# Kernel tuning notes

Measured on AMD Instinct MI355X. Metric: run time of the kernel, lower is better.

## Reference

```python
import jax, jax.numpy as jnp
import numpy as np
from jax import lax

DN = ('NDHWC', 'DHWIO', 'NDHWC')
SHAPE = (33, 33, 33)
B = 2
N = 40000
C = 64


def setup_inputs() -> dict:
    key = jax.random.key(0)
    ks = jax.random.split(key, 24)
    D, H, W = SHAPE
    # unique active voxel coords (batch, z, y, x)
    rng = np.random.default_rng(0)
    idx = rng.choice(B * D * H * W, size=N, replace=False)
    b = idx // (D * H * W)
    r = idx % (D * H * W)
    coors = np.stack([b, r // (H * W), (r // W) % H, r % W], axis=1).astype(np.int32)

    def w(k, shape, scale=0.1):
        return jax.random.normal(k, shape, jnp.float32) * scale

    inp = {
        'features': jax.random.normal(ks[0], (N, 3), jnp.float32),
        'coors': jnp.asarray(coors),
        'batch_size': B,
        'w1': w(ks[1], (3, 3, 3, 3, C), 0.2), 'b1': w(ks[2], (C,), 0.05),
        'w2': w(ks[3], (3, 3, 3, C, C), 0.05), 'b2': w(ks[4], (C,), 0.05),
        'w3': w(ks[5], (3, 3, 3, C, C), 0.05), 'b3': w(ks[6], (C,), 0.05),
        'wt': w(ks[7], (3, 3, 3, C, C), 0.05), 'bt': w(ks[8], (C,), 0.05),
        'w5': w(ks[9], (3, 3, 3, C, C), 0.05), 'b5': w(ks[10], (C,), 0.05),
    }
    # folded eval-mode BatchNorm: y = x*s + h  (s = gamma/sqrt(var+eps), h = beta - mean*s)
    for i, (sk, hk) in enumerate(zip(ks[11:16], ks[16:21]), start=1):
        inp[f's{i}'] = 1.0 + 0.1 * jax.random.normal(sk, (C,), jnp.float32)
        inp[f'h{i}'] = 0.05 * jax.random.normal(hk, (C,), jnp.float32)
    return inp


def _forward(features, coors, batch_size,
             w1, b1, w2, b2, w3, b3, wt, bt, w5, b5,
             s1, h1, s2, h2, s3, h3, s4, h4, s5, h5):
    D, H, W = SHAPE
    bi, zi, yi, xi = coors[:, 0], coors[:, 1], coors[:, 2], coors[:, 3]
    # densify SparseConvTensor (zeros at inactive sites) + active mask
    x = jnp.zeros((batch_size, D, H, W, features.shape[-1]), features.dtype)
    x = x.at[bi, zi, yi, xi].set(features)
    m = jnp.zeros((batch_size, D, H, W, 1), jnp.float32).at[bi, zi, yi, xi].set(1.0)
    ones3 = jnp.ones((3, 3, 3, 1, 1), jnp.float32)

    conv = lambda a, k, pad: lax.conv_general_dilated(a, k, (1, 1, 1), pad, dimension_numbers=DN)
    # masked BN(eval) + ReLU: applied only on active sites, background stays exactly 0
    act = lambda y, mm, s, h: jnp.where(mm, jax.nn.relu(y * s + h), 0.0)

    # SparseConv3d(3,64,3): valid conv; output actives = 1-dilation of input actives
    x = conv(x, w1, 'VALID')
    m1 = conv(m, ones3, 'VALID') > 0  # [B,31,31,31,1]
    x = act(x + b1, m1, s1, h1)

    # two SubMConv3d(64,64,3) sharing indice_key: same active set, SAME padding
    x = act(conv(x, w2, 'SAME') + b2, m1, s2, h2)
    x = act(conv(x, w3, 'SAME') + b3, m1, s3, h3)

    # SparseConvTranspose3d(64,64,3,2): out = (D-1)*2+3; actives = transposed dilation
    x = lax.conv_transpose(x, wt, (2, 2, 2), 'VALID', dimension_numbers=DN)
    mT = lax.conv_transpose(m1.astype(jnp.float32), ones3, (2, 2, 2), 'VALID', dimension_numbers=DN) > 0
    x = act(x + bt, mT, s4, h4)

    # ToDense -> dense Conv3d(64,64,3) -> BN -> ReLU (dense: applied everywhere)
    x = conv(x, w5, 'VALID') + b5
    x = jax.nn.relu(x * s5 + h5)
    return jnp.transpose(x, (0, 4, 1, 2, 3))  # NCDHW like spconv ToDense output


def reference(features, coors, batch_size,
              w1, b1, w2, b2, w3, b3, wt, bt, w5, b5,
              s1, h1, s2, h2, s3, h3, s4, h4, s5, h5):
    return _forward(features, coors, batch_size,
                    w1, b1, w2, b2, w3, b3, wt, bt, w5, b5,
                    s1, h1, s2, h2, s3, h3, s4, h4, s5, h5)
```

## Files before the change

### kernel.cpp

```cpp
#include <hip/hip_runtime.h>
#include <cstdint>

constexpr int BB = 2, C = 64;
constexpr int D1 = 31;
constexpr int DP = 33;
constexpr int D4 = 63;
constexpr int D5 = 61;
constexpr int D5CUBE = D5*D5*D5;

constexpr int NV1 = BB*D1*D1*D1;
constexpr int NVP = BB*DP*DP*DP;
constexpr int NV4 = BB*D4*D4*D4;
constexpr int NV5 = BB*D5*D5*D5;

constexpr size_t alup(size_t x) { return (x + 255) & ~(size_t)255; }
constexpr size_t OB_X0  = 0;
constexpr size_t OB_M0  = alup(OB_X0  + (size_t)NVP*3*4);
constexpr size_t OB_M1P = alup(OB_M0  + (size_t)NVP*4);
constexpr size_t OB_X1  = alup(OB_M1P + (size_t)NVP*4);
constexpr size_t OB_X2  = alup(OB_X1  + (size_t)NVP*64*2);
constexpr size_t OB_X3  = alup(OB_X2  + (size_t)NVP*64*2);
constexpr size_t OB_MT  = alup(OB_X3  + (size_t)NVP*64*2);
constexpr size_t OB_X4  = alup(OB_MT  + (size_t)NV4*4);
constexpr size_t OB_WB2 = alup(OB_X4  + (size_t)NV4*64*2);
constexpr size_t OB_WB3 = alup(OB_WB2 + (size_t)27*64*64*2);
constexpr size_t OB_WBT = alup(OB_WB3 + (size_t)27*64*64*2);
constexpr size_t OB_WB5 = alup(OB_WBT + (size_t)27*64*64*2);

typedef __attribute__((ext_vector_type(8))) short short8;
typedef __attribute__((ext_vector_type(4))) float f32x4;

__device__ inline unsigned short f2bf(float f) {
  unsigned int u = __float_as_uint(f);
  u = (u + 0x7FFFu + ((u >> 16) & 1u)) >> 16;
  return (unsigned short)u;
}

template<int DD>
__device__ inline void decodev(int vox, int& b, int& z, int& y, int& x) {
  x = vox % DD; int r = vox / DD;
  y = r % DD;   r /= DD;
  z = r % DD;   b = r / DD;
}

__device__ inline int xcd_swz(int bid, int nb) {
  int q = nb >> 3, r = nb & 7;
  int xcd = bid & 7, idx = bid >> 3;
  return (xcd < r ? xcd*(q+1) : r*(q+1) + (xcd - r)*q) + idx;
}

__global__ void k_scatter(const float* __restrict__ feat, const int* __restrict__ coors,
                          int n, float* __restrict__ x0, float* __restrict__ m0) {
  int i = blockIdx.x*blockDim.x + threadIdx.x;
  if (i >= n) return;
  int b = coors[4*i+0], z = coors[4*i+1], y = coors[4*i+2], x = coors[4*i+3];
  int v = ((b*DP + z)*DP + y)*DP + x;
  x0[v*3+0] = feat[3*i+0];
  x0[v*3+1] = feat[3*i+1];
  x0[v*3+2] = feat[3*i+2];
  m0[v] = 1.0f;
}

__global__ void __launch_bounds__(256)
k_conv1(const float* __restrict__ x0, const float* __restrict__ m0,
        unsigned short* __restrict__ x1, float* __restrict__ m1p,
        const float* __restrict__ w1, const float* __restrict__ b1,
        const float* __restrict__ s1, const float* __restrict__ h1) {
  long long t = (long long)blockIdx.x*blockDim.x + threadIdx.x;
  if (t >= (long long)NV1*C) return;
  int co  = (int)(t & 63);
  int vox = (int)(t >> 6);
  int b, z, y, x; decodev<D1>(vox, b, z, y, x);
  float sum = 0.f, mm = 0.f;
  #pragma unroll
  for (int kz=0; kz<3; kz++)
  #pragma unroll
  for (int ky=0; ky<3; ky++)
  #pragma unroll
  for (int kx=0; kx<3; kx++) {
    int iv = ((b*DP + z+kz)*DP + y+ky)*DP + (x+kx);
    mm += m0[iv];
    const float* px = x0 + iv*3;
    const float* pw = w1 + ((kz*3+ky)*3+kx)*3*64 + co;
    sum += px[0]*pw[0] + px[1]*pw[64] + px[2]*pw[128];
  }
  bool m = mm > 0.f;
  float o = m ? fmaxf((sum + b1[co])*s1[co] + h1[co], 0.f) : 0.f;
  size_t pOff = (size_t)(((b*DP + z+1)*DP + y+1)*DP + (x+1));
  x1[pOff*C + co] = f2bf(o);
  if (co == 0) m1p[pOff] = m ? 1.f : 0.f;
}

__global__ void k_repack4(const float* __restrict__ wa, const float* __restrict__ wb,
                          const float* __restrict__ wc, const float* __restrict__ wd,
                          unsigned short* __restrict__ da, unsigned short* __restrict__ db,
                          unsigned short* __restrict__ dc, unsigned short* __restrict__ dd) {
  int which = blockIdx.x / 432;
  int i = (blockIdx.x - which*432)*256 + threadIdx.x;
  const float* w = which == 0 ? wa : which == 1 ? wb : which == 2 ? wc : wd;
  unsigned short* dst = which == 0 ? da : which == 1 ? db : which == 2 ? dc : dd;
  int co = i & 63, k = (i >> 6) & 63, t = i >> 12;
  int kk = k >> 5, q = (k >> 3) & 3, j = k & 7, cb = co >> 4, l = q*16 + (co & 15);
  dst[(size_t)((t*2+kk)*4+cb)*512 + l*8 + j] = f2bf(w[i]);
}

template<int NA, int DOUT, int DIN>
__global__ void __launch_bounds__(256)
k_conv_mfma(const unsigned short* __restrict__ inBF, const unsigned short* __restrict__ wB,
            unsigned short* __restrict__ outPtr, const float* __restrict__ m1p,
            const float* __restrict__ bias, const float* __restrict__ s,
            const float* __restrict__ h) {
  constexpr int NVOX = BB*DOUT*DOUT*DOUT;
  const int lane = threadIdx.x & 63;
  const int wid  = threadIdx.x >> 6;
  const int wave = xcd_swz(blockIdx.x, gridDim.x)*4 + wid;
  const int vb   = wave * (NA*16);

  int rowb[NA];
  #pragma unroll
  for (int a = 0; a < NA; a++) {
    int vox = vb + a*16 + (lane & 15);
    vox = vox < NVOX ? vox : NVOX-1;
    int b, z, y, x; decodev<DOUT>(vox, b, z, y, x);
    rowb[a] = (((b*DIN + z)*DIN + y)*DIN + x)*64;
  }
  const int koff = (lane >> 4) * 8;

  f32x4 acc[NA][4];
  #pragma unroll
  for (int a = 0; a < NA; a++)
    #pragma unroll
    for (int cb = 0; cb < 4; cb++)
      acc[a][cb] = f32x4{0.f, 0.f, 0.f, 0.f};

  #pragma unroll 1
  for (int t = 0; t < 27; ++t) {
    int kz = t / 9, rr = t - kz*9;
    int ky = rr / 3, kx = rr - ky*3;
    const int toff = ((kz*DIN + ky)*DIN + kx)*64;
    #pragma unroll
    for (int kk = 0; kk < 2; ++kk) {
      short8 A[NA];
      #pragma unroll
      for (int a = 0; a < NA; a++)
        A[a] = *reinterpret_cast<const short8*>(inBF + rowb[a] + toff + kk*32 + koff);
      short8 Bv[4];
      const unsigned short* wp = wB + (size_t)(t*2+kk)*2048 + lane*8;
      #pragma unroll
      for (int cb = 0; cb < 4; cb++)
        Bv[cb] = *reinterpret_cast<const short8*>(wp + cb*512);
      #pragma unroll
      for (int a = 0; a < NA; a++)
        #pragma unroll
        for (int cb = 0; cb < 4; cb++)
          acc[a][cb] = __builtin_amdgcn_mfma_f32_16x16x32_bf16(A[a], Bv[cb], acc[a][cb], 0, 0, 0);
    }
  }

  float bv[4], sv[4], hv[4];
  #pragma unroll
  for (int cb = 0; cb < 4; cb++) {
    int c = cb*16 + (lane & 15);
    bv[cb] = bias[c]; sv[cb] = s[c]; hv[cb] = h[c];
  }

  #pragma unroll
  for (int a = 0; a < NA; a++)
    #pragma unroll
    for (int r = 0; r < 4; r++) {
      int vox = vb + a*16 + (lane >> 4)*4 + r;
      if (vox >= NVOX) continue;
      int b, z, y, x; decodev<DOUT>(vox, b, z, y, x);
      size_t pOff = (size_t)(((b*DP + z+1)*DP + y+1)*DP + (x+1));
      bool m = m1p[pOff] > 0.f;
      #pragma unroll
      for (int cb = 0; cb < 4; cb++) {
        float o = m ? fmaxf((acc[a][cb][r] + bv[cb])*sv[cb] + hv[cb], 0.f) : 0.f;
        outPtr[pOff*64 + cb*16 + (lane & 15)] = f2bf(o);
      }
    }
}

__global__ void __launch_bounds__(256)
k_maskT(const float* __restrict__ m1p, float* __restrict__ mt) {
  int vox = blockIdx.x*256 + threadIdx.x;
  if (vox >= NV4) return;
  int b, zo, yo, xo; decodev<D4>(vox, b, zo, yo, xo);
  float mm = 0.f;
  for (int kz = 0; kz < 3; kz++) {
    if ((zo + kz) & 1) continue;
    int izp = ((zo + kz - 2) >> 1) + 1;
    for (int ky = 0; ky < 3; ky++) {
      if ((yo + ky) & 1) continue;
      int iyp = ((yo + ky - 2) >> 1) + 1;
      for (int kx = 0; kx < 3; kx++) {
        if ((xo + kx) & 1) continue;
        int ixp = ((xo + kx - 2) >> 1) + 1;
        mm += m1p[((b*DP + izp)*DP + iyp)*DP + ixp];
      }
    }
  }
  mt[vox] = mm;
}

__global__ void __launch_bounds__(256)
k_convT_mfma(const unsigned short* __restrict__ x3, const unsigned short* __restrict__ wB,
             unsigned short* __restrict__ x4, const float* __restrict__ mt,
             const float* __restrict__ bias, const float* __restrict__ s,
             const float* __restrict__ h) {
  const int lane = threadIdx.x & 63;
  const int wid  = threadIdx.x >> 6;
  const int w    = xcd_swz(blockIdx.x, gridDim.x)*4 + wid;
  if (w >= BB*D4*D4) return;
  const int b  = w / (D4*D4);
  const int rm = w % (D4*D4);
  const int zo = rm / D4;
  const int yo = rm % D4;
  const int ii = lane & 15;
  const int koff = (lane >> 4) * 8;

  f32x4 acc[4][4];
  #pragma unroll
  for (int a = 0; a < 4; a++)
    #pragma unroll
    for (int cb = 0; cb < 4; cb++)
      acc[a][cb] = f32x4{0.f, 0.f, 0.f, 0.f};

  #pragma unroll 1
  for (int kz = 0; kz < 3; kz++) {
    if ((zo + kz) & 1) continue;
    const int izp = ((zo + kz - 2) >> 1) + 1;
    #pragma unroll 1
    for (int ky = 0; ky < 3; ky++) {
      if ((yo + ky) & 1) continue;
      const int iyp = ((yo + ky - 2) >> 1) + 1;
      const size_t planeBase = ((size_t)((b*DP + izp)*DP + iyp))*DP*64;
      #pragma unroll
      for (int kx = 0; kx < 3; kx++) {
        const int apar  = kx & 1;
        const int xoffE = ((kx + apar - 2) >> 1) + 1;
        const int t = (kz*3 + ky)*3 + kx;
        #pragma unroll
        for (int kk = 0; kk < 2; ++kk) {
          short8 Bv[4];
          const unsigned short* wpk = wB + (size_t)(t*2+kk)*2048 + lane*8;
          #pragma unroll
          for (int cb = 0; cb < 4; cb++)
            Bv[cb] = *reinterpret_cast<const short8*>(wpk + cb*512);
          #pragma unroll
          for (int ablk = 0; ablk < 2; ablk++) {
            const int ixp = ablk*16 + ii + xoffE;
            short8 A = *reinterpret_cast<const short8*>(x3 + planeBase + (size_t)ixp*64 + kk*32 + koff);
            const int afr = apar*2 + ablk;
            #pragma unroll
            for (int cb = 0; cb < 4; cb++)
              acc[afr][cb] = __builtin_amdgcn_mfma_f32_16x16x32_bf16(A, Bv[cb], acc[afr][cb], 0, 0, 0);
          }
        }
      }
    }
  }

  float bv[4], sv[4], hv[4];
  #pragma unroll
  for (int cb = 0; cb < 4; cb++) {
    int c = cb*16 + (lane & 15);
    bv[cb] = bias[c]; sv[cb] = s[c]; hv[cb] = h[c];
  }
  const int rowBase = ((b*D4 + zo)*D4 + yo)*D4;
  #pragma unroll
  for (int a = 0; a < 4; a++) {
    const int ablk = a & 1, apar = a >> 1;
    #pragma unroll
    for (int r = 0; r < 4; r++) {
      const int row = (lane >> 4)*4 + r;
      const int xo  = 2*(ablk*16 + row) + apar;
      if (xo >= D4) continue;
      const int vox = rowBase + xo;
      const bool m = mt[vox] > 0.f;
      #pragma unroll
      for (int cb = 0; cb < 4; cb++) {
        float o = m ? fmaxf((acc[a][cb][r] + bv[cb])*sv[cb] + hv[cb], 0.f) : 0.f;
        x4[(size_t)vox*64 + cb*16 + (lane & 15)] = f2bf(o);
      }
    }
  }
}

__device__ __forceinline__ void c5_step(const short8 (&A)[4], const short8 (&W)[4],
                                        f32x4 (&acc)[4][4]) {
  #pragma unroll
  for (int a = 0; a < 4; a++)
    #pragma unroll
    for (int cb = 0; cb < 4; cb++)
      acc[a][cb] = __builtin_amdgcn_mfma_f32_16x16x32_bf16(W[cb], A[a], acc[a][cb], 0, 0, 0);
}

__global__ void __launch_bounds__(256, 2)
k_conv5_mfma(const unsigned short* __restrict__ x4, const unsigned short* __restrict__ wB,
             float* __restrict__ out, const float* __restrict__ bias,
             const float* __restrict__ s, const float* __restrict__ h) {
  __shared__ short8 sbuf[2][2048];
  const int tid  = threadIdx.x;
  const int lane = tid & 63;
  const int wid  = tid >> 6;
  const int ll   = lane & 15;
  const int l16  = lane >> 4;

  const int blk   = xcd_swz(blockIdx.x, gridDim.x);
  const int ytile = blk & 15;
  const int rzb   = blk >> 4;
  const int z     = rzb % D5;
  const int b     = rzb / D5;
  const int y0    = ytile * 4;

  int st_r[8], st_base[8];
  #pragma unroll
  for (int it = 0; it < 8; ++it) {
    int g = it*256 + tid; g = g > 2015 ? 2015 : g;
    int r = g / 504, rem = g - r*504;
    int v = rem >> 3, c16p = rem & 7;
    int c16l = c16p ^ (v & 7);
    st_r[it] = r;
    st_base[it] = (v << 7) + (c16l << 4);
  }

  const char* x4b = (const char*)x4;

  f32x4 acc[4][4];
  #pragma unroll
  for (int a = 0; a < 4; a++)
    #pragma unroll
    for (int cb = 0; cb < 4; cb++)
      acc[a][cb] = f32x4{0.f, 0.f, 0.f, 0.f};

  auto STAGE = [&](int kzn, int kyn, int hn) {
    size_t pb = (size_t)(b*D4 + z + kzn) * (D4*D4*128);
    char* dst = (char*)&sbuf[hn][0];
    #pragma unroll
    for (int it = 0; it < 8; ++it) {
      int yin = y0 + st_r[it] + kyn; yin = yin > 62 ? 62 : yin;
      __builtin_amdgcn_global_load_lds(
        (const __attribute__((address_space(1))) void*)(x4b + pb + (size_t)yin*8064 + st_base[it]),
        (__attribute__((address_space(3))) void*)(dst + it*4096 + wid*1024),
        16, 0, 0);
    }
  };
  auto LDA = [&](int hh, int kx, int kk, short8 (&A)[4]) {
    #pragma unroll
    for (int a = 0; a < 4; a++) {
      int v  = a*16 + ll + kx;
      int ch = wid*504 + v*8 + ((kk*4 + l16) ^ (v & 7));
      A[a] = sbuf[hh][ch];
    }
  };
  auto LDW = [&](int slot, short8 (&W)[4]) {
    const unsigned short* wp = wB + (size_t)slot*2048 + lane*8;
    #pragma unroll
    for (int cb = 0; cb < 4; cb++)
      W[cb] = *reinterpret_cast<const short8*>(wp + cb*512);
  };

  short8 A0[4], A1[4], W0[4], W1[4];

  STAGE(0, 0, 0);
  LDW(0, W0);
  __syncthreads();

  int kzn = 0, kyn = 1;
  #pragma unroll 1
  for (int p = 0; p < 9; ++p) {
    const int hh = p & 1;
    if (p < 8) {
      STAGE(kzn, kyn, hh ^ 1);
      kyn++; if (kyn == 3) { kyn = 0; kzn++; }
    }
    LDA(hh, 0, 0, A0);
    const int sbase = p*6;
    #pragma unroll
    for (int st = 0; st < 6; ++st) {
      const int kxn = (st+1) >> 1, kkn = (st+1) & 1;
      if (st < 5) {
        if (st & 1) LDA(hh, kxn, kkn, A0); else LDA(hh, kxn, kkn, A1);
      }
      if (sbase + st + 1 < 54) {
        if (st & 1) LDW(sbase + st + 1, W0); else LDW(sbase + st + 1, W1);
      }
      if (st & 1) c5_step(A1, W1, acc); else c5_step(A0, W0, acc);
    }
    __syncthreads();
  }

  const int yout = y0 + wid;
  if (yout < D5) {
    #pragma unroll
    for (int a = 0; a < 4; a++) {
      int x = a*16 + ll;
      if (x >= D5) continue;
      size_t sp = (size_t)(z*D5 + yout)*D5 + x;
      #pragma unroll
      for (int cb = 0; cb < 4; cb++)
        #pragma unroll
        for (int r = 0; r < 4; r++) {
          int co = cb*16 + l16*4 + r;
          float o = fmaxf((acc[a][cb][r] + bias[co])*s[co] + h[co], 0.f);
          out[(size_t)(b*64 + co)*D5CUBE + sp] = o;
        }
    }
  }
}

extern "C" void kernel_launch(void* const* d_in, const int* in_sizes, int n_in,
                              void* d_out, int out_size, void* d_ws, size_t ws_size,
                              hipStream_t stream) {
  const float* feat  = (const float*)d_in[0];
  const int*   coors = (const int*)d_in[1];
  const float* w1 = (const float*)d_in[3];
  const float* b1 = (const float*)d_in[4];
  const float* w2 = (const float*)d_in[5];
  const float* b2 = (const float*)d_in[6];
  const float* w3 = (const float*)d_in[7];
  const float* b3 = (const float*)d_in[8];
  const float* wt = (const float*)d_in[9];
  const float* bt = (const float*)d_in[10];
  const float* w5 = (const float*)d_in[11];
  const float* b5 = (const float*)d_in[12];
  const float* s1 = (const float*)d_in[13];
  const float* h1 = (const float*)d_in[14];
  const float* s2 = (const float*)d_in[15];
  const float* h2 = (const float*)d_in[16];
  const float* s3 = (const float*)d_in[17];
  const float* h3 = (const float*)d_in[18];
  const float* s4 = (const float*)d_in[19];
  const float* h4 = (const float*)d_in[20];
  const float* s5 = (const float*)d_in[21];
  const float* h5 = (const float*)d_in[22];
  int n = in_sizes[0] / 3;

  char* wsb = (char*)d_ws;
  float*          X0  = (float*)(wsb + OB_X0);
  float*          M0  = (float*)(wsb + OB_M0);
  float*          M1P = (float*)(wsb + OB_M1P);
  unsigned short* X1  = (unsigned short*)(wsb + OB_X1);
  unsigned short* X2  = (unsigned short*)(wsb + OB_X2);
  unsigned short* X3  = (unsigned short*)(wsb + OB_X3);
  float*          MT  = (float*)(wsb + OB_MT);
  unsigned short* X4  = (unsigned short*)(wsb + OB_X4);
  unsigned short* WB2 = (unsigned short*)(wsb + OB_WB2);
  unsigned short* WB3 = (unsigned short*)(wsb + OB_WB3);
  unsigned short* WBT = (unsigned short*)(wsb + OB_WBT);
  unsigned short* WB5 = (unsigned short*)(wsb + OB_WB5);

  hipMemsetAsync(wsb, 0, OB_MT, stream);

  k_repack4<<<1728, 256, 0, stream>>>(w2, w3, wt, w5, WB2, WB3, WBT, WB5);

  k_scatter<<<(n+255)/256, 256, 0, stream>>>(feat, coors, n, X0, M0);

  {
    long long threads = (long long)NV1*C;
    k_conv1<<<(int)((threads+255)/256), 256, 0, stream>>>(X0, M0, X1, M1P, w1, b1, s1, h1);
  }

  constexpr int WAVES23 = (NV1 + 31) / 32;
  constexpr int BLK23   = (WAVES23 + 3) / 4;
  k_conv_mfma<2, D1, DP><<<BLK23, 256, 0, stream>>>(X1, WB2, X2, M1P, b2, s2, h2);
  k_conv_mfma<2, D1, DP><<<BLK23, 256, 0, stream>>>(X2, WB3, X3, M1P, b3, s3, h3);

  k_maskT<<<(NV4 + 255)/256, 256, 0, stream>>>(M1P, MT);

  constexpr int ROWS_T = BB*D4*D4;
  k_convT_mfma<<<(ROWS_T + 3)/4, 256, 0, stream>>>(X3, WBT, X4, MT, bt, s4, h4);

  constexpr int BLK5 = BB * D5 * 16;
  k_conv5_mfma<<<BLK5, 256, 0, stream>>>(X4, WB5, (float*)d_out, b5, s5, h5);
}
```

Measured before the change: 372.2 us.

## Stage conv5 weights through LDS and zero only padded halo borders

In the final dense conv kernel, each pipeline stage's weight slab is now loaded into a double-buffered LDS array with async global-to-LDS copies alongside the activation tile, and MFMA operands are read from LDS instead of directly from global memory. The launch-bounds occupancy hint is dropped because LDS use grows. Separately, the full workspace memset is replaced by a kernel that zeros the masks and input features everywhere but clears the bf16 activation buffers only on the padded boundary voxels, relying on the interior being fully overwritten. This cuts memset traffic and per-wave global weight loads, at the cost of more LDS and possibly lower occupancy.

```diff
diff --git a/kernel.cpp b/kernel.cpp
--- a/kernel.cpp
+++ b/kernel.cpp
@@ -47,6 +47,27 @@
   int q = nb >> 3, r = nb & 7;
   int xcd = bid & 7, idx = bid >> 3;
   return (xcd < r ? xcd*(q+1) : r*(q+1) + (xcd - r)*q) + idx;
+}
+
+__global__ void __launch_bounds__(256)
+k_zero(float* __restrict__ x0, float* __restrict__ m0, float* __restrict__ m1p,
+       unsigned short* __restrict__ x1, unsigned short* __restrict__ x2,
+       unsigned short* __restrict__ x3) {
+  int v = blockIdx.x*256 + threadIdx.x;
+  if (v >= NVP) return;
+  m0[v] = 0.f; m1p[v] = 0.f;
+  x0[3*v+0] = 0.f; x0[3*v+1] = 0.f; x0[3*v+2] = 0.f;
+  int x = v % DP, r = v / DP;
+  int y = r % DP; r /= DP;
+  int z = r % DP;
+  if (x==0 || x==DP-1 || y==0 || y==DP-1 || z==0 || z==DP-1) {
+    ulonglong2 zz = {0ull, 0ull};
+    ulonglong2* p1 = (ulonglong2*)(x1 + (size_t)v*64);
+    ulonglong2* p2 = (ulonglong2*)(x2 + (size_t)v*64);
+    ulonglong2* p3 = (ulonglong2*)(x3 + (size_t)v*64);
+    #pragma unroll
+    for (int i = 0; i < 8; i++) { p1[i] = zz; p2[i] = zz; p3[i] = zz; }
+  }
 }
 
 __global__ void k_scatter(const float* __restrict__ feat, const int* __restrict__ coors,
@@ -296,11 +317,12 @@
       acc[a][cb] = __builtin_amdgcn_mfma_f32_16x16x32_bf16(W[cb], A[a], acc[a][cb], 0, 0, 0);
 }
 
-__global__ void __launch_bounds__(256, 2)
+__global__ void __launch_bounds__(256)
 k_conv5_mfma(const unsigned short* __restrict__ x4, const unsigned short* __restrict__ wB,
              float* __restrict__ out, const float* __restrict__ bias,
              const float* __restrict__ s, const float* __restrict__ h) {
-  __shared__ short8 sbuf[2][2048];
+  __shared__ short8 sA[2][2048];
+  __shared__ short8 sW[2][1536];
   const int tid  = threadIdx.x;
   const int lane = tid & 63;
   const int wid  = tid >> 6;
@@ -326,6 +348,7 @@
   }
 
   const char* x4b = (const char*)x4;
+  const char* wBb = (const char*)wB;
 
   f32x4 acc[4][4];
   #pragma unroll
@@ -334,9 +357,9 @@
     for (int cb = 0; cb < 4; cb++)
       acc[a][cb] = f32x4{0.f, 0.f, 0.f, 0.f};
 
-  auto STAGE = [&](int kzn, int kyn, int hn) {
+  auto STAGE_A = [&](int kzn, int kyn, int hn) {
     size_t pb = (size_t)(b*D4 + z + kzn) * (D4*D4*128);
-    char* dst = (char*)&sbuf[hn][0];
+    char* dst = (char*)&sA[hn][0];
     #pragma unroll
     for (int it = 0; it < 8; ++it) {
       int yin = y0 + st_r[it] + kyn; yin = yin > 62 ? 62 : yin;
@@ -346,25 +369,35 @@
         16, 0, 0);
     }
   };
+  auto STAGE_W = [&](int pn, int hn) {
+    const char* src = wBb + (size_t)pn*24576;
+    char* dst = (char*)&sW[hn][0];
+    #pragma unroll
+    for (int it = 0; it < 6; ++it) {
+      __builtin_amdgcn_global_load_lds(
+        (const __attribute__((address_space(1))) void*)(src + it*4096 + tid*16),
+        (__attribute__((address_space(3))) void*)(dst + it*4096 + wid*1024),
+        16, 0, 0);
+    }
+  };
   auto LDA = [&](int hh, int kx, int kk, short8 (&A)[4]) {
     #pragma unroll
     for (int a = 0; a < 4; a++) {
       int v  = a*16 + ll + kx;
       int ch = wid*504 + v*8 + ((kk*4 + l16) ^ (v & 7));
-      A[a] = sbuf[hh][ch];
+      A[a] = sA[hh][ch];
     }
   };
-  auto LDW = [&](int slot, short8 (&W)[4]) {
-    const unsigned short* wp = wB + (size_t)slot*2048 + lane*8;
+  auto LDW = [&](int hh, int st, short8 (&W)[4]) {
     #pragma unroll
     for (int cb = 0; cb < 4; cb++)
-      W[cb] = *reinterpret_cast<const short8*>(wp + cb*512);
+      W[cb] = sW[hh][st*256 + cb*64 + lane];
   };
 
   short8 A0[4], A1[4], W0[4], W1[4];
 
-  STAGE(0, 0, 0);
-  LDW(0, W0);
+  STAGE_A(0, 0, 0);
+  STAGE_W(0, 0);
   __syncthreads();
 
   int kzn = 0, kyn = 1;
@@ -372,19 +405,18 @@
   for (int p = 0; p < 9; ++p) {
     const int hh = p & 1;
     if (p < 8) {
-      STAGE(kzn, kyn, hh ^ 1);
+      STAGE_A(kzn, kyn, hh ^ 1);
+      STAGE_W(p + 1, hh ^ 1);
       kyn++; if (kyn == 3) { kyn = 0; kzn++; }
     }
     LDA(hh, 0, 0, A0);
-    const int sbase = p*6;
+    LDW(hh, 0, W0);
     #pragma unroll
     for (int st = 0; st < 6; ++st) {
       const int kxn = (st+1) >> 1, kkn = (st+1) & 1;
       if (st < 5) {
-        if (st & 1) LDA(hh, kxn, kkn, A0); else LDA(hh, kxn, kkn, A1);
-      }
-      if (sbase + st + 1 < 54) {
-        if (st & 1) LDW(sbase + st + 1, W0); else LDW(sbase + st + 1, W1);
+        if (st & 1) { LDA(hh, kxn, kkn, A0); LDW(hh, st+1, W0); }
+        else        { LDA(hh, kxn, kkn, A1); LDW(hh, st+1, W1); }
       }
       if (st & 1) c5_step(A1, W1, acc); else c5_step(A0, W0, acc);
     }
@@ -451,7 +483,7 @@
   unsigned short* WBT = (unsigned short*)(wsb + OB_WBT);
   unsigned short* WB5 = (unsigned short*)(wsb + OB_WB5);
 
-  hipMemsetAsync(wsb, 0, OB_MT, stream);
+  k_zero<<<(NVP + 255)/256, 256, 0, stream>>>(X0, M0, M1P, X1, X2, X3);
 
   k_repack4<<<1728, 256, 0, stream>>>(w2, w3, wt, w5, WB2, WB3, WBT, WB5);
 
```

After: 405.6 us. +9.0%, slower.
